# Optimization experiments

Hardware: AMD Instinct MI355X
Metric: run time of the kernel (lower is better)

Reference implementation:

```python
import jax, jax.numpy as jnp
import numpy as np

N = 50000
E = 800000
NUM_KINDS = 100
D_NODE = 64
D_EDGE = 4
D_MSG = 64
L = 3
D_IN = 2 * D_NODE + D_EDGE  # 132


def setup_inputs() -> dict:
    key = jax.random.key(0)
    ks = jax.random.split(key, 20)

    def w(k, shape, fan_in):
        bound = 1.0 / np.sqrt(fan_in)
        return jax.random.uniform(k, shape, jnp.float32, -bound, bound)

    inp = {
        "edge_index": jax.random.randint(ks[0], (2, E), 0, N),
        "node_kind_ids": jax.random.randint(ks[1], (N,), 0, NUM_KINDS),
        "edge_attr": jax.random.normal(ks[2], (E, D_EDGE), jnp.float32),
        # learned params
        "emb": jax.random.normal(ks[3], (NUM_KINDS, D_NODE), jnp.float32),
        # stacked per-layer message MLP params [L, ...]
        "msg_w1": w(ks[4], (L, D_MSG, D_IN), D_IN),
        "msg_b1": w(ks[5], (L, D_MSG), D_IN),
        "msg_w2": w(ks[6], (L, D_MSG, D_MSG), D_MSG),
        "msg_b2": w(ks[7], (L, D_MSG), D_MSG),
        # stacked per-layer GRUCell params (torch layout: [3*d_node, d_in])
        "gru_wih": w(ks[8], (L, 3 * D_NODE, D_MSG), D_NODE),
        "gru_whh": w(ks[9], (L, 3 * D_NODE, D_NODE), D_NODE),
        "gru_bih": w(ks[10], (L, 3 * D_NODE), D_NODE),
        "gru_bhh": w(ks[11], (L, 3 * D_NODE), D_NODE),
        # edge head: Linear(132,64) -> SiLU -> Linear(64,1)
        "head_w1": w(ks[12], (64, D_IN), D_IN),
        "head_b1": w(ks[13], (64,), D_IN),
        "head_w2": w(ks[14], (1, 64), 64),
        "head_b2": w(ks[15], (1,), 64),
    }
    return inp


def reference(edge_index, node_kind_ids, edge_attr, emb,
              msg_w1, msg_b1, msg_w2, msg_b2,
              gru_wih, gru_whh, gru_bih, gru_bhh,
              head_w1, head_b1, head_w2, head_b2):
    src, dst = edge_index[0], edge_index[1]
    h = emb[node_kind_ids]  # [N, d_node]
    n_nodes = h.shape[0]
    for l in range(L):
        x = jnp.concatenate([h[src], h[dst], edge_attr], axis=1)  # [E, 132]
        m = jax.nn.silu(x @ msg_w1[l].T + msg_b1[l]) @ msg_w2[l].T + msg_b2[l]  # [E, d_msg]
        agg = jax.ops.segment_sum(m, dst, num_segments=n_nodes)  # [N, d_msg]
        # torch GRUCell math
        gi = agg @ gru_wih[l].T + gru_bih[l]  # [N, 3*d_node]
        gh = h @ gru_whh[l].T + gru_bhh[l]
        ir, iz, inn = jnp.split(gi, 3, axis=1)
        hr, hz, hn = jnp.split(gh, 3, axis=1)
        r = jax.nn.sigmoid(ir + hr)
        z = jax.nn.sigmoid(iz + hz)
        n = jnp.tanh(inn + r * hn)
        h = (1.0 - z) * n + z * h
    x = jnp.concatenate([h[src], h[dst], edge_attr], axis=1)  # [E, 132]
    logits = (jax.nn.silu(x @ head_w1.T + head_b1) @ head_w2.T + head_b2)[:, 0]
    return jax.nn.sigmoid(logits)  # [E]
```

## Files before the change

### kernel.cpp

```cpp
#include <hip/hip_runtime.h>
#include <hip/hip_bf16.h>


typedef __attribute__((ext_vector_type(8))) short bf16x8;
typedef __attribute__((ext_vector_type(4))) float f32x4;
#define MFMA16(a, b, c) __builtin_amdgcn_mfma_f32_16x16x32_bf16(a, b, c, 0, 0, 0)

#define CHUNK 128
#define XSTRIDE 336
#define MSTRIDE 264
#define HSTRIDE 144
#define SLABSZ 10752
#define HIDSZ  4608

#define WRZST 264
#define WNST  136

__device__ __forceinline__ float fast_sig(float x) { return 1.f / (1.f + __expf(-x)); }
__device__ __forceinline__ float fast_tanh(float x) {
    float ax = fabsf(x);
    float t = __expf(-2.f * ax);
    return copysignf((1.f - t) / (1.f + t), x);
}
__device__ __forceinline__ ushort f2bf(float f) {
    unsigned u = __float_as_uint(f);
    unsigned r = u + 0x7FFF + ((u >> 16) & 1);
    return (ushort)(r >> 16);
}
__device__ __forceinline__ float bf2f(ushort b) {
    return __uint_as_float(((unsigned)b) << 16);
}
__device__ __forceinline__ unsigned pkbf2(float a, float b) {
    unsigned r;
    asm("v_cvt_pk_bf16_f32 %0, %1, %2" : "=v"(r) : "v"(a), "v"(b));
    return r;
}

__global__ void prep_kernel(const float* __restrict__ msg_w1,
                            const float* __restrict__ msg_b1,
                            const float* __restrict__ msg_w2,
                            const float* __restrict__ gru_wih,
                            const float* __restrict__ gru_whh,
                            const float* __restrict__ head_w1,
                            const float* __restrict__ head_b1,
                            const float* __restrict__ head_w2,
                            ushort* __restrict__ Wb1, ushort* __restrict__ Wb2,
                            ushort* __restrict__ Wh1, ushort* __restrict__ Wh2b,
                            ushort* __restrict__ Wrz, ushort* __restrict__ Wni,
                            ushort* __restrict__ Wnh) {
    int t = blockIdx.x * 256 + threadIdx.x;
    if (t < 30720) {
        int l = t / 10240, r = t % 10240, j = r / 160, k = r % 160;
        float v = 0.f;
        if (k < 132) {
            v = msg_w1[l * 8448 + j * 132 + k];
        } else if (k == 132) {
            v = msg_b1[l * 64 + j];
        } else if (k == 133) {
            float b = msg_b1[l * 64 + j];
            v = b - bf2f(f2bf(b));
        }
        Wb1[t] = f2bf(v);
        return;
    }
    t -= 30720;
    if (t < 12288) {
        Wb2[t] = f2bf(msg_w2[t]);
        return;
    }
    t -= 12288;
    if (t < 10240) {
        int j = t / 160, k = t % 160;
        float v = 0.f;
        if (k < 132) {
            v = head_w1[j * 132 + k];
        } else if (k == 132) {
            v = head_b1[j];
        } else if (k == 133) {
            float b = head_b1[j];
            v = b - bf2f(f2bf(b));
        }
        Wh1[t] = f2bf(v);
        return;
    }
    t -= 10240;
    if (t < 1024) {
        int j = t >> 6, k = t & 63;
        Wh2b[t] = (j == 0) ? f2bf(head_w2[k]) : 0;
        return;
    }
    t -= 1024;
    if (t < 49152) {
        int l = t / 16384, r = t % 16384, n = r >> 7, k = r & 127;
        float v = (k < 64) ? gru_wih[l * 12288 + n * 64 + k]
                           : gru_whh[l * 12288 + n * 64 + (k - 64)];
        Wrz[t] = f2bf(v);
        return;
    }
    t -= 49152;
    if (t < 12288) {
        int l = t / 4096, r = t % 4096, j = r >> 6, k = r & 63;
        Wni[t] = f2bf(gru_wih[l * 12288 + (128 + j) * 64 + k]);
        return;
    }
    t -= 12288;
    if (t < 12288) {
        int l = t / 4096, r = t % 4096, j = r >> 6, k = r & 63;
        Wnh[t] = f2bf(gru_whh[l * 12288 + (128 + j) * 64 + k]);
    }
}

__global__ void embed_kernel(float* __restrict__ h, ushort* __restrict__ hb,
                             const float* __restrict__ emb,
                             const int* __restrict__ kinds, int N) {
    int t = blockIdx.x * 256 + threadIdx.x;
    if (t >= N * 64) return;
    int node = t >> 6, d = t & 63;
    float v = emb[kinds[node] * 64 + d];
    h[t] = v;
    hb[t] = f2bf(v);
}

__global__ void hist_kernel(const int* __restrict__ dst, int* __restrict__ deg, int E) {
    int e = blockIdx.x * 256 + threadIdx.x;
    if (e < E) atomicAdd(&deg[dst[e]], 1);
}

__global__ void scan_kernel(const int* __restrict__ deg, int* __restrict__ cursor, int N) {
    __shared__ int sums[1024];
    int tid = threadIdx.x;
    int chunk = (N + 1023) >> 10;
    int lo = tid * chunk, hi = min(lo + chunk, N);
    int s = 0;
    for (int i = lo; i < hi; i++) s += deg[i];
    sums[tid] = s;
    __syncthreads();
    for (int off = 1; off < 1024; off <<= 1) {
        int v = (tid >= off) ? sums[tid - off] : 0;
        __syncthreads();
        sums[tid] += v;
        __syncthreads();
    }
    int run = (tid > 0) ? sums[tid - 1] : 0;
    for (int i = lo; i < hi; i++) {
        cursor[i] = run;
        run += deg[i];
    }
}

__global__ void scatter_kernel(const int* __restrict__ src, const int* __restrict__ dst,
                               const float* __restrict__ ea, int* __restrict__ cursor,
                               int* __restrict__ src_s, int* __restrict__ dst_s,
                               ushort* __restrict__ ea_sb, int E) {
    int e = blockIdx.x * 256 + threadIdx.x;
    if (e >= E) return;
    int d = dst[e];
    int p = atomicAdd(&cursor[d], 1);
    src_s[p] = src[e];
    dst_s[p] = d;
    float4 e4 = ((const float4*)ea)[e];
    ushort4 eb;
    eb.x = f2bf(e4.x); eb.y = f2bf(e4.y); eb.z = f2bf(e4.z); eb.w = f2bf(e4.w);
    ((ushort4*)ea_sb)[p] = eb;
}

__global__ __launch_bounds__(256) void edge_msg_mfma(
    const ushort* __restrict__ hb, const int* __restrict__ src_s,
    const int* __restrict__ dst_s, const ushort* __restrict__ ea_sb,
    const ushort* __restrict__ Wb1l, const ushort* __restrict__ Wb2l,
    const float* __restrict__ b2,
    float* __restrict__ agg, int E, int nchunks) {
    __shared__ char lds[4 * SLABSZ + 4 * HIDSZ];
    int tid = threadIdx.x;
    int w = tid >> 6, lane = tid & 63;
    int quad = lane >> 4, nrow = lane & 15;
    char* slab = lds + w * SLABSZ;
    char* hidb = lds + 4 * SLABSZ + w * HIDSZ;

    bf16x8 wf1[4][5], wf2[4][2];
    float b2v[4];
#pragma unroll
    for (int nt = 0; nt < 4; nt++) {
        int n = nt * 16 + nrow;
#pragma unroll
        for (int ks = 0; ks < 5; ks++)
            wf1[nt][ks] = *(const bf16x8*)(Wb1l + n * 160 + ks * 32 + quad * 8);
#pragma unroll
        for (int ks = 0; ks < 2; ks++)
            wf2[nt][ks] = *(const bf16x8*)(Wb2l + n * 64 + ks * 32 + quad * 8);
        b2v[nt] = b2[n];
    }

    for (int chunk = blockIdx.x; chunk < nchunks; chunk += gridDim.x) {
        int ebase = chunk * CHUNK;
        {
            int el = tid >> 1, half = tid & 1;
            int r = el & 31;
            int ec = min(ebase + el, E - 1);
            int node = half ? dst_s[ec] : src_s[ec];
            const float4* hrow = (const float4*)(hb + (size_t)node * 64);
            float4* xw = (float4*)(slab + r * XSTRIDE + half * 128);
#pragma unroll
            for (int i = 0; i < 8; i++) xw[i] = hrow[i];
            if (half == 0) {
                *(uint2*)(slab + r * XSTRIDE + 256) = *(const uint2*)(ea_sb + (size_t)ec * 4);
            } else {
                uint2 ones2 = {0x3F803F80u, 0u};
                float4 z4 = {0.f, 0.f, 0.f, 0.f};
                *(uint2*)(slab + r * XSTRIDE + 264) = ones2;
                *(float4*)(slab + r * XSTRIDE + 272) = z4;
                *(float4*)(slab + r * XSTRIDE + 288) = z4;
                *(float4*)(slab + r * XSTRIDE + 304) = z4;
            }
        }
        f32x4 acc1[4][2];
#pragma unroll
        for (int nt = 0; nt < 4; nt++) {
            f32x4 z4;
            z4[0] = z4[1] = z4[2] = z4[3] = 0.f;
            acc1[nt][0] = z4;
            acc1[nt][1] = z4;
        }
#pragma unroll
        for (int ks = 0; ks < 5; ks++) {
            bf16x8 xb0 = *(const bf16x8*)(slab + nrow * XSTRIDE + ks * 64 + quad * 16);
            bf16x8 xb1 = *(const bf16x8*)(slab + (16 + nrow) * XSTRIDE + ks * 64 + quad * 16);
#pragma unroll
            for (int nt = 0; nt < 4; nt++) {
                acc1[nt][0] = MFMA16(wf1[nt][ks], xb0, acc1[nt][0]);
                acc1[nt][1] = MFMA16(wf1[nt][ks], xb1, acc1[nt][1]);
            }
        }
#pragma unroll
        for (int nt = 0; nt < 4; nt++)
#pragma unroll
            for (int et = 0; et < 2; et++) {
                f32x4 a = acc1[nt][et];
                float v0 = a[0] * fast_sig(a[0]);
                float v1 = a[1] * fast_sig(a[1]);
                float v2 = a[2] * fast_sig(a[2]);
                float v3 = a[3] * fast_sig(a[3]);
                int er = et * 16 + nrow;
                uint2 pk;
                pk.x = pkbf2(v0, v1);
                pk.y = pkbf2(v2, v3);
                *(uint2*)(hidb + er * HSTRIDE + nt * 32 + quad * 8) = pk;
            }
        f32x4 acc2[2][4];
#pragma unroll
        for (int mt = 0; mt < 2; mt++)
#pragma unroll
            for (int nt = 0; nt < 4; nt++) {
                f32x4 v;
                v[0] = v[1] = v[2] = v[3] = b2v[nt];
                acc2[mt][nt] = v;
            }
#pragma unroll
        for (int ks = 0; ks < 2; ks++) {
            bf16x8 a0 = *(const bf16x8*)(hidb + nrow * HSTRIDE + ks * 64 + quad * 16);
            bf16x8 a1 = *(const bf16x8*)(hidb + (16 + nrow) * HSTRIDE + ks * 64 + quad * 16);
#pragma unroll
            for (int nt = 0; nt < 4; nt++) {
                acc2[0][nt] = MFMA16(a0, wf2[nt][ks], acc2[0][nt]);
                acc2[1][nt] = MFMA16(a1, wf2[nt][ks], acc2[1][nt]);
            }
        }
#pragma unroll
        for (int mt = 0; mt < 2; mt++)
#pragma unroll
            for (int nt = 0; nt < 4; nt++)
#pragma unroll
                for (int rg = 0; rg < 4; rg++) {
                    int rm = mt * 16 + quad * 4 + rg;
                    *(float*)(slab + rm * MSTRIDE + (nt * 16 + nrow) * 4) = acc2[mt][nt][rg];
                }
        {
            int e32 = ebase + w * 32;
            int dmy = dst_s[min(e32 + (lane & 31), E - 1)];
            int limit = min(32, E - e32);
            int nx = __shfl_down(dmy, 1);
            bool tl = ((lane & 31) == 31) || (dmy != nx);
            unsigned long long tm = __ballot(tl);
            float run = 0.f;
#pragma unroll
            for (int i = 0; i < 32; i++) {
                if (i < limit) {
                    run += *(const float*)(slab + i * MSTRIDE + lane * 4);
                    if (((tm >> i) & 1ull) || (i + 1 == limit)) {
                        int di = __shfl(dmy, i);
                        unsafeAtomicAdd(&agg[(size_t)di * 64 + lane], run);
                        run = 0.f;
                    }
                }
            }
        }
    }
}

__global__ __launch_bounds__(256) void head_mfma(
    const ushort* __restrict__ hb, const int* __restrict__ src,
    const int* __restrict__ dst, const float* __restrict__ ea,
    const ushort* __restrict__ Wh1, const ushort* __restrict__ Wh2b,
    const float* __restrict__ hb2p,
    float* __restrict__ out, int E, int nchunks) {
    __shared__ char lds[4 * SLABSZ + 4 * HIDSZ];
    int tid = threadIdx.x;
    int w = tid >> 6, lane = tid & 63;
    int quad = lane >> 4, nrow = lane & 15;
    char* slab = lds + w * SLABSZ;
    char* hidb = lds + 4 * SLABSZ + w * HIDSZ;

    bf16x8 wf1[4][5], wh2[2];
#pragma unroll
    for (int nt = 0; nt < 4; nt++) {
        int n = nt * 16 + nrow;
#pragma unroll
        for (int ks = 0; ks < 5; ks++)
            wf1[nt][ks] = *(const bf16x8*)(Wh1 + n * 160 + ks * 32 + quad * 8);
    }
#pragma unroll
    for (int ks = 0; ks < 2; ks++)
        wh2[ks] = *(const bf16x8*)(Wh2b + nrow * 64 + ks * 32 + quad * 8);
    float hb2 = hb2p[0];

    for (int chunk = blockIdx.x; chunk < nchunks; chunk += gridDim.x) {
        int ebase = chunk * CHUNK;
        {
            int el = tid >> 1, half = tid & 1;
            int r = el & 31;
            int ec = min(ebase + el, E - 1);
            int node = half ? dst[ec] : src[ec];
            const float4* hrow = (const float4*)(hb + (size_t)node * 64);
            float4* xw = (float4*)(slab + r * XSTRIDE + half * 128);
#pragma unroll
            for (int i = 0; i < 8; i++) xw[i] = hrow[i];
            if (half == 0) {
                float4 e4 = ((const float4*)ea)[ec];
                ushort4 eb;
                eb.x = f2bf(e4.x); eb.y = f2bf(e4.y); eb.z = f2bf(e4.z); eb.w = f2bf(e4.w);
                *(ushort4*)(slab + r * XSTRIDE + 256) = eb;
            } else {
                uint2 ones2 = {0x3F803F80u, 0u};
                float4 z4 = {0.f, 0.f, 0.f, 0.f};
                *(uint2*)(slab + r * XSTRIDE + 264) = ones2;
                *(float4*)(slab + r * XSTRIDE + 272) = z4;
                *(float4*)(slab + r * XSTRIDE + 288) = z4;
                *(float4*)(slab + r * XSTRIDE + 304) = z4;
            }
        }
        f32x4 acc1[4][2];
#pragma unroll
        for (int nt = 0; nt < 4; nt++) {
            f32x4 z4;
            z4[0] = z4[1] = z4[2] = z4[3] = 0.f;
            acc1[nt][0] = z4;
            acc1[nt][1] = z4;
        }
#pragma unroll
        for (int ks = 0; ks < 5; ks++) {
            bf16x8 xb0 = *(const bf16x8*)(slab + nrow * XSTRIDE + ks * 64 + quad * 16);
            bf16x8 xb1 = *(const bf16x8*)(slab + (16 + nrow) * XSTRIDE + ks * 64 + quad * 16);
#pragma unroll
            for (int nt = 0; nt < 4; nt++) {
                acc1[nt][0] = MFMA16(wf1[nt][ks], xb0, acc1[nt][0]);
                acc1[nt][1] = MFMA16(wf1[nt][ks], xb1, acc1[nt][1]);
            }
        }
#pragma unroll
        for (int nt = 0; nt < 4; nt++)
#pragma unroll
            for (int et = 0; et < 2; et++) {
                f32x4 a = acc1[nt][et];
                float v0 = a[0] * fast_sig(a[0]);
                float v1 = a[1] * fast_sig(a[1]);
                float v2 = a[2] * fast_sig(a[2]);
                float v3 = a[3] * fast_sig(a[3]);
                int er = et * 16 + nrow;
                uint2 pk;
                pk.x = pkbf2(v0, v1);
                pk.y = pkbf2(v2, v3);
                *(uint2*)(hidb + er * HSTRIDE + nt * 32 + quad * 8) = pk;
            }
        f32x4 acc3[2];
#pragma unroll
        for (int mt = 0; mt < 2; mt++) {
            f32x4 v;
            v[0] = v[1] = v[2] = v[3] = 0.f;
            acc3[mt] = v;
        }
#pragma unroll
        for (int ks = 0; ks < 2; ks++) {
            bf16x8 a0 = *(const bf16x8*)(hidb + nrow * HSTRIDE + ks * 64 + quad * 16);
            bf16x8 a1 = *(const bf16x8*)(hidb + (16 + nrow) * HSTRIDE + ks * 64 + quad * 16);
            acc3[0] = MFMA16(a0, wh2[ks], acc3[0]);
            acc3[1] = MFMA16(a1, wh2[ks], acc3[1]);
        }
        if (nrow == 0) {
#pragma unroll
            for (int mt = 0; mt < 2; mt++)
#pragma unroll
                for (int rg = 0; rg < 4; rg++) {
                    int e = ebase + w * 32 + mt * 16 + quad * 4 + rg;
                    if (e < E) out[e] = fast_sig(acc3[mt][rg] + hb2);
                }
        }
    }
}

__device__ __forceinline__ bf16x8 aggfrag(const float* __restrict__ row, int off) {
    float4 f0 = *(const float4*)(row + off);
    float4 f1 = *(const float4*)(row + off + 4);
    bf16x8 r;
    r[0] = (short)f2bf(f0.x); r[1] = (short)f2bf(f0.y);
    r[2] = (short)f2bf(f0.z); r[3] = (short)f2bf(f0.w);
    r[4] = (short)f2bf(f1.x); r[5] = (short)f2bf(f1.y);
    r[6] = (short)f2bf(f1.z); r[7] = (short)f2bf(f1.w);
    return r;
}

__global__ __launch_bounds__(256) void gru_mfma(
    float* __restrict__ h, ushort* __restrict__ hb, const float* __restrict__ agg,
    const ushort* __restrict__ Wrzg, const ushort* __restrict__ Wnig,
    const ushort* __restrict__ Wnhg,
    const float* __restrict__ bih, const float* __restrict__ bhh, int N) {
    __shared__ char lds[128 * WRZST + 2 * 64 * WNST];
    int tid = threadIdx.x, w = tid >> 6, lane = tid & 63;
    int quad = lane >> 4, nrow = lane & 15;
    char* wrz = lds;
    char* wni = lds + 128 * WRZST;
    char* wnh = wni + 64 * WNST;

    {
        int r = tid >> 1, half = tid & 1;
        const uint4* g = (const uint4*)(Wrzg + r * 128 + half * 64);
        uint4* d = (uint4*)(wrz + r * WRZST + half * 128);
#pragma unroll
        for (int i = 0; i < 8; i++) d[i] = g[i];
        if (tid < 128) {
            const uint4* g2 = (const uint4*)(Wnig + (tid >> 1) * 64 + (tid & 1) * 32);
            uint4* d2 = (uint4*)(wni + (tid >> 1) * WNST + (tid & 1) * 64);
#pragma unroll
            for (int i = 0; i < 4; i++) d2[i] = g2[i];
        } else {
            int t2 = tid - 128;
            const uint4* g2 = (const uint4*)(Wnhg + (t2 >> 1) * 64 + (t2 & 1) * 32);
            uint4* d2 = (uint4*)(wnh + (t2 >> 1) * WNST + (t2 & 1) * 64);
#pragma unroll
            for (int i = 0; i < 4; i++) d2[i] = g2[i];
        }
    }
    __syncthreads();

    int nb0 = blockIdx.x * 128 + w * 32;
    if (nb0 >= N) return;

    float brz[8], bi[4], bhv[4];
#pragma unroll
    for (int nt = 0; nt < 8; nt++) brz[nt] = bih[nt * 16 + nrow] + bhh[nt * 16 + nrow];
#pragma unroll
    for (int nt = 0; nt < 4; nt++) {
        bi[nt] = bih[128 + nt * 16 + nrow];
        bhv[nt] = bhh[128 + nt * 16 + nrow];
    }

    int n0 = min(nb0 + nrow, N - 1);
    int n1 = min(nb0 + 16 + nrow, N - 1);
    const float* ag0 = agg + (size_t)n0 * 64;
    const float* ag1 = agg + (size_t)n1 * 64;
    const ushort* hb0 = hb + (size_t)n0 * 64;
    const ushort* hb1 = hb + (size_t)n1 * 64;

    f32x4 accrz[2][8], acci[2][4], acch[2][4];
#pragma unroll
    for (int nt = 0; nt < 8; nt++) {
        f32x4 v; v[0] = v[1] = v[2] = v[3] = brz[nt];
        accrz[0][nt] = v; accrz[1][nt] = v;
    }
#pragma unroll
    for (int nt = 0; nt < 4; nt++) {
        f32x4 vi; vi[0] = vi[1] = vi[2] = vi[3] = bi[nt];
        acci[0][nt] = vi; acci[1][nt] = vi;
        f32x4 vh; vh[0] = vh[1] = vh[2] = vh[3] = bhv[nt];
        acch[0][nt] = vh; acch[1][nt] = vh;
    }

#pragma unroll
    for (int ks = 0; ks < 4; ks++) {
        bf16x8 a0, a1;
        if (ks < 2) {
            a0 = aggfrag(ag0, ks * 32 + quad * 8);
            a1 = aggfrag(ag1, ks * 32 + quad * 8);
        } else {
            a0 = *(const bf16x8*)(hb0 + (ks - 2) * 32 + quad * 8);
            a1 = *(const bf16x8*)(hb1 + (ks - 2) * 32 + quad * 8);
        }
#pragma unroll
        for (int nt = 0; nt < 8; nt++) {
            bf16x8 b = *(const bf16x8*)(wrz + (nt * 16 + nrow) * WRZST + ks * 64 + quad * 16);
            accrz[0][nt] = MFMA16(a0, b, accrz[0][nt]);
            accrz[1][nt] = MFMA16(a1, b, accrz[1][nt]);
        }
        if (ks < 2) {
#pragma unroll
            for (int nt = 0; nt < 4; nt++) {
                bf16x8 b = *(const bf16x8*)(wni + (nt * 16 + nrow) * WNST + ks * 64 + quad * 16);
                acci[0][nt] = MFMA16(a0, b, acci[0][nt]);
                acci[1][nt] = MFMA16(a1, b, acci[1][nt]);
            }
        } else {
#pragma unroll
            for (int nt = 0; nt < 4; nt++) {
                bf16x8 b = *(const bf16x8*)(wnh + (nt * 16 + nrow) * WNST + (ks - 2) * 64 + quad * 16);
                acch[0][nt] = MFMA16(a0, b, acch[0][nt]);
                acch[1][nt] = MFMA16(a1, b, acch[1][nt]);
            }
        }
    }

#pragma unroll
    for (int mt = 0; mt < 2; mt++)
#pragma unroll
        for (int nt = 0; nt < 4; nt++)
#pragma unroll
            for (int rg = 0; rg < 4; rg++) {
                int node = nb0 + mt * 16 + quad * 4 + rg;
                if (node < N) {
                    int col = nt * 16 + nrow;
                    float r = fast_sig(accrz[mt][nt][rg]);
                    float z = fast_sig(accrz[mt][nt + 4][rg]);
                    float nn = fast_tanh(acci[mt][nt][rg] + r * acch[mt][nt][rg]);
                    size_t idx = (size_t)node * 64 + col;
                    float ho = h[idx];
                    float hnew = (1.f - z) * nn + z * ho;
                    h[idx] = hnew;
                    hb[idx] = f2bf(hnew);
                }
            }
}

extern "C" void kernel_launch(void* const* d_in, const int* in_sizes, int n_in,
                              void* d_out, int out_size, void* d_ws, size_t ws_size,
                              hipStream_t stream) {
    const int* edge_index = (const int*)d_in[0];
    int E = in_sizes[0] / 2;
    const int* src = edge_index;
    const int* dst = edge_index + E;
    const int* kinds = (const int*)d_in[1];
    int N = in_sizes[1];
    const float* edge_attr = (const float*)d_in[2];
    const float* emb = (const float*)d_in[3];
    const float* msg_w1 = (const float*)d_in[4];
    const float* msg_b1 = (const float*)d_in[5];
    const float* msg_w2 = (const float*)d_in[6];
    const float* msg_b2 = (const float*)d_in[7];
    const float* gru_wih = (const float*)d_in[8];
    const float* gru_whh = (const float*)d_in[9];
    const float* gru_bih = (const float*)d_in[10];
    const float* gru_bhh = (const float*)d_in[11];
    const float* head_w1 = (const float*)d_in[12];
    const float* head_b1 = (const float*)d_in[13];
    const float* head_w2 = (const float*)d_in[14];
    const float* head_b2 = (const float*)d_in[15];
    float* out = (float*)d_out;

    char* p = (char*)d_ws;
    float* h = (float*)p;        p += (size_t)N * 64 * 4;
    float* agg = (float*)p;      p += (size_t)N * 64 * 4;
    int* deg = (int*)p;          p += (size_t)N * 4;
    int* cursor = (int*)p;       p += (size_t)N * 4;
    int* src_s = (int*)p;        p += (size_t)E * 4;
    int* dst_s = (int*)p;        p += (size_t)E * 4;
    ushort* hb = (ushort*)p;     p += (size_t)N * 64 * 2;
    ushort* Wb1 = (ushort*)p;    p += 30720 * 2;
    ushort* Wb2 = (ushort*)p;    p += 12288 * 2;
    ushort* Wh1 = (ushort*)p;    p += 10240 * 2;
    ushort* Wh2b = (ushort*)p;   p += 1024 * 2;
    ushort* Wrz = (ushort*)p;    p += 49152 * 2;
    ushort* Wni = (ushort*)p;    p += 12288 * 2;
    ushort* Wnh = (ushort*)p;    p += 12288 * 2;
    ushort* ea_sb = (ushort*)p;  p += (size_t)E * 4 * 2;

    int nchunks = (E + CHUNK - 1) / CHUNK;

    prep_kernel<<<500, 256, 0, stream>>>(msg_w1, msg_b1, msg_w2, gru_wih, gru_whh,
                                         head_w1, head_b1, head_w2,
                                         Wb1, Wb2, Wh1, Wh2b, Wrz, Wni, Wnh);
    embed_kernel<<<(N * 64 + 255) / 256, 256, 0, stream>>>(h, hb, emb, kinds, N);

    hipMemsetAsync(deg, 0, (size_t)N * sizeof(int), stream);
    hist_kernel<<<(E + 255) / 256, 256, 0, stream>>>(dst, deg, E);
    scan_kernel<<<1, 1024, 0, stream>>>(deg, cursor, N);
    scatter_kernel<<<(E + 255) / 256, 256, 0, stream>>>(src, dst, edge_attr, cursor,
                                                        src_s, dst_s, ea_sb, E);

    for (int l = 0; l < 3; l++) {
        hipMemsetAsync(agg, 0, (size_t)N * 64 * sizeof(float), stream);
        edge_msg_mfma<<<512, 256, 0, stream>>>(
            hb, src_s, dst_s, ea_sb,
            Wb1 + l * 10240, Wb2 + l * 4096,
            msg_b2 + l * 64, agg, E, nchunks);
        gru_mfma<<<(N + 127) / 128, 256, 0, stream>>>(
            h, hb, agg, Wrz + l * 16384, Wni + l * 4096, Wnh + l * 4096,
            gru_bih + l * 192, gru_bhh + l * 192, N);
    }
    head_mfma<<<512, 256, 0, stream>>>(hb, src, dst, edge_attr, Wh1, Wh2b,
                                       head_b2, out, E, nchunks);
}
```

Baseline: 671.6 us.

## Raise edge-kernel occupancy by reusing LDS slab and reloading second-layer weights

Result: slower. 706.1 us (+5.1%).

```diff
diff --git a/kernel.cpp b/kernel.cpp
--- a/kernel.cpp
+++ b/kernel.cpp
@@ -11,7 +11,6 @@
 #define MSTRIDE 264
 #define HSTRIDE 144
 #define SLABSZ 10752
-#define HIDSZ  4608
 
 #define WRZST 264
 #define WNST  136
@@ -164,20 +163,19 @@
     ((ushort4*)ea_sb)[p] = eb;
 }
 
-__global__ __launch_bounds__(256) void edge_msg_mfma(
+__global__ __launch_bounds__(256, 3) void edge_msg_mfma(
     const ushort* __restrict__ hb, const int* __restrict__ src_s,
     const int* __restrict__ dst_s, const ushort* __restrict__ ea_sb,
     const ushort* __restrict__ Wb1l, const ushort* __restrict__ Wb2l,
     const float* __restrict__ b2,
     float* __restrict__ agg, int E, int nchunks) {
-    __shared__ char lds[4 * SLABSZ + 4 * HIDSZ];
+    __shared__ char lds[4 * SLABSZ];
     int tid = threadIdx.x;
     int w = tid >> 6, lane = tid & 63;
     int quad = lane >> 4, nrow = lane & 15;
     char* slab = lds + w * SLABSZ;
-    char* hidb = lds + 4 * SLABSZ + w * HIDSZ;
-
-    bf16x8 wf1[4][5], wf2[4][2];
+
+    bf16x8 wf1[4][5];
     float b2v[4];
 #pragma unroll
     for (int nt = 0; nt < 4; nt++) {
@@ -185,9 +183,6 @@
 #pragma unroll
         for (int ks = 0; ks < 5; ks++)
             wf1[nt][ks] = *(const bf16x8*)(Wb1l + n * 160 + ks * 32 + quad * 8);
-#pragma unroll
-        for (int ks = 0; ks < 2; ks++)
-            wf2[nt][ks] = *(const bf16x8*)(Wb2l + n * 64 + ks * 32 + quad * 8);
         b2v[nt] = b2[n];
     }
 
@@ -213,13 +208,12 @@
                 *(float4*)(slab + r * XSTRIDE + 304) = z4;
             }
         }
-        f32x4 acc1[4][2];
-#pragma unroll
-        for (int nt = 0; nt < 4; nt++) {
+        f32x4 acc[8];
+        {
             f32x4 z4;
             z4[0] = z4[1] = z4[2] = z4[3] = 0.f;
-            acc1[nt][0] = z4;
-            acc1[nt][1] = z4;
+#pragma unroll
+            for (int i = 0; i < 8; i++) acc[i] = z4;
         }
 #pragma unroll
         for (int ks = 0; ks < 5; ks++) {
@@ -227,15 +221,15 @@
             bf16x8 xb1 = *(const bf16x8*)(slab + (16 + nrow) * XSTRIDE + ks * 64 + quad * 16);
 #pragma unroll
             for (int nt = 0; nt < 4; nt++) {
-                acc1[nt][0] = MFMA16(wf1[nt][ks], xb0, acc1[nt][0]);
-                acc1[nt][1] = MFMA16(wf1[nt][ks], xb1, acc1[nt][1]);
+                acc[nt * 2 + 0] = MFMA16(wf1[nt][ks], xb0, acc[nt * 2 + 0]);
+                acc[nt * 2 + 1] = MFMA16(wf1[nt][ks], xb1, acc[nt * 2 + 1]);
             }
         }
 #pragma unroll
         for (int nt = 0; nt < 4; nt++)
 #pragma unroll
             for (int et = 0; et < 2; et++) {
-                f32x4 a = acc1[nt][et];
+                f32x4 a = acc[nt * 2 + et];
                 float v0 = a[0] * fast_sig(a[0]);
                 float v1 = a[1] * fast_sig(a[1]);
                 float v2 = a[2] * fast_sig(a[2]);
@@ -244,27 +238,40 @@
                 uint2 pk;
                 pk.x = pkbf2(v0, v1);
                 pk.y = pkbf2(v2, v3);
-                *(uint2*)(hidb + er * HSTRIDE + nt * 32 + quad * 8) = pk;
-            }
-        f32x4 acc2[2][4];
+                *(uint2*)(slab + er * HSTRIDE + nt * 32 + quad * 8) = pk;
+            }
+        bf16x8 ha[2][2];
+#pragma unroll
+        for (int mt = 0; mt < 2; mt++)
+#pragma unroll
+            for (int ks = 0; ks < 2; ks++) {
+                int er = mt * 16 + nrow;
+                ha[mt][ks] = *(const bf16x8*)(slab + er * HSTRIDE + ks * 64 + quad * 16);
+            }
+        const ushort* wb2i = Wb2l;
+        asm volatile("" : "+s"(wb2i));
+        bf16x8 wf2[4][2];
+#pragma unroll
+        for (int nt = 0; nt < 4; nt++)
+#pragma unroll
+            for (int ks = 0; ks < 2; ks++)
+                wf2[nt][ks] =
+                    *(const bf16x8*)(wb2i + (nt * 16 + nrow) * 64 + ks * 32 + quad * 8);
 #pragma unroll
         for (int mt = 0; mt < 2; mt++)
 #pragma unroll
             for (int nt = 0; nt < 4; nt++) {
                 f32x4 v;
                 v[0] = v[1] = v[2] = v[3] = b2v[nt];
-                acc2[mt][nt] = v;
-            }
-#pragma unroll
-        for (int ks = 0; ks < 2; ks++) {
-            bf16x8 a0 = *(const bf16x8*)(hidb + nrow * HSTRIDE + ks * 64 + quad * 16);
-            bf16x8 a1 = *(const bf16x8*)(hidb + (16 + nrow) * HSTRIDE + ks * 64 + quad * 16);
+                acc[mt * 4 + nt] = v;
+            }
+#pragma unroll
+        for (int ks = 0; ks < 2; ks++)
 #pragma unroll
             for (int nt = 0; nt < 4; nt++) {
-                acc2[0][nt] = MFMA16(a0, wf2[nt][ks], acc2[0][nt]);
-                acc2[1][nt] = MFMA16(a1, wf2[nt][ks], acc2[1][nt]);
-            }
-        }
+                acc[0 * 4 + nt] = MFMA16(ha[0][ks], wf2[nt][ks], acc[0 * 4 + nt]);
+                acc[1 * 4 + nt] = MFMA16(ha[1][ks], wf2[nt][ks], acc[1 * 4 + nt]);
+            }
 #pragma unroll
         for (int mt = 0; mt < 2; mt++)
 #pragma unroll
@@ -272,7 +279,8 @@
 #pragma unroll
                 for (int rg = 0; rg < 4; rg++) {
                     int rm = mt * 16 + quad * 4 + rg;
-                    *(float*)(slab + rm * MSTRIDE + (nt * 16 + nrow) * 4) = acc2[mt][nt][rg];
+                    *(float*)(slab + rm * MSTRIDE + (nt * 16 + nrow) * 4) =
+                        acc[mt * 4 + nt][rg];
                 }
         {
             int e32 = ebase + w * 32;
@@ -297,20 +305,19 @@
     }
 }
 
-__global__ __launch_bounds__(256) void head_mfma(
+__global__ __launch_bounds__(256, 3) void head_mfma(
     const ushort* __restrict__ hb, const int* __restrict__ src,
     const int* __restrict__ dst, const float* __restrict__ ea,
     const ushort* __restrict__ Wh1, const ushort* __restrict__ Wh2b,
     const float* __restrict__ hb2p,
     float* __restrict__ out, int E, int nchunks) {
-    __shared__ char lds[4 * SLABSZ + 4 * HIDSZ];
+    __shared__ char lds[4 * SLABSZ];
     int tid = threadIdx.x;
     int w = tid >> 6, lane = tid & 63;
     int quad = lane >> 4, nrow = lane & 15;
     char* slab = lds + w * SLABSZ;
-    char* hidb = lds + 4 * SLABSZ + w * HIDSZ;
-
-    bf16x8 wf1[4][5], wh2[2];
+
+    bf16x8 wf1[4][5];
 #pragma unroll
     for (int nt = 0; nt < 4; nt++) {
         int n = nt * 16 + nrow;
@@ -318,9 +325,6 @@
         for (int ks = 0; ks < 5; ks++)
             wf1[nt][ks] = *(const bf16x8*)(Wh1 + n * 160 + ks * 32 + quad * 8);
     }
-#pragma unroll
-    for (int ks = 0; ks < 2; ks++)
-        wh2[ks] = *(const bf16x8*)(Wh2b + nrow * 64 + ks * 32 + quad * 8);
     float hb2 = hb2p[0];
 
     for (int chunk = blockIdx.x; chunk < nchunks; chunk += gridDim.x) {
@@ -348,13 +352,12 @@
                 *(float4*)(slab + r * XSTRIDE + 304) = z4;
             }
         }
-        f32x4 acc1[4][2];
-#pragma unroll
-        for (int nt = 0; nt < 4; nt++) {
+        f32x4 acc[8];
+        {
             f32x4 z4;
             z4[0] = z4[1] = z4[2] = z4[3] = 0.f;
-            acc1[nt][0] = z4;
-            acc1[nt][1] = z4;
+#pragma unroll
+            for (int i = 0; i < 8; i++) acc[i] = z4;
         }
 #pragma unroll
         for (int ks = 0; ks < 5; ks++) {
@@ -362,15 +365,15 @@
             bf16x8 xb1 = *(const bf16x8*)(slab + (16 + nrow) * XSTRIDE + ks * 64 + quad * 16);
 #pragma unroll
             for (int nt = 0; nt < 4; nt++) {
-                acc1[nt][0] = MFMA16(wf1[nt][ks], xb0, acc1[nt][0]);
-                acc1[nt][1] = MFMA16(wf1[nt][ks], xb1, acc1[nt][1]);
+                acc[nt * 2 + 0] = MFMA16(wf1[nt][ks], xb0, acc[nt * 2 + 0]);
+                acc[nt * 2 + 1] = MFMA16(wf1[nt][ks], xb1, acc[nt * 2 + 1]);
             }
         }
 #pragma unroll
         for (int nt = 0; nt < 4; nt++)
 #pragma unroll
             for (int et = 0; et < 2; et++) {
-                f32x4 a = acc1[nt][et];
+                f32x4 a = acc[nt * 2 + et];
                 float v0 = a[0] * fast_sig(a[0]);
                 float v1 = a[1] * fast_sig(a[1]);
                 float v2 = a[2] * fast_sig(a[2]);
@@ -379,8 +382,23 @@
                 uint2 pk;
                 pk.x = pkbf2(v0, v1);
                 pk.y = pkbf2(v2, v3);
-                *(uint2*)(hidb + er * HSTRIDE + nt * 32 + quad * 8) = pk;
-            }
+                *(uint2*)(slab + er * HSTRIDE + nt * 32 + quad * 8) = pk;
+            }
+        bf16x8 ha[2][2];
+#pragma unroll
+        for (int mt = 0; mt < 2; mt++)
+#pragma unroll
+            for (int ks = 0; ks < 2; ks++) {
+                int er = mt * 16 + nrow;
+                ha[mt][ks] = *(const bf16x8*)(slab + er * HSTRIDE + ks * 64 + quad * 16);
+            }
+        const ushort* wh2i = Wh2b;
+        asm volatile("" : "+s"(wh2i));
+        bf16x8 wh2[2];
+#pragma unroll
+        for (int ks = 0; ks < 2; ks++)
+            wh2[ks] = *(const bf16x8*)(wh2i + nrow * 64 + ks * 32 + quad * 8);
+
         f32x4 acc3[2];
 #pragma unroll
         for (int mt = 0; mt < 2; mt++) {
@@ -390,10 +408,8 @@
         }
 #pragma unroll
         for (int ks = 0; ks < 2; ks++) {
-            bf16x8 a0 = *(const bf16x8*)(hidb + nrow * HSTRIDE + ks * 64 + quad * 16);
-            bf16x8 a1 = *(const bf16x8*)(hidb + (16 + nrow) * HSTRIDE + ks * 64 + quad * 16);
-            acc3[0] = MFMA16(a0, wh2[ks], acc3[0]);
-            acc3[1] = MFMA16(a1, wh2[ks], acc3[1]);
+            acc3[0] = MFMA16(ha[0][ks], wh2[ks], acc3[0]);
+            acc3[1] = MFMA16(ha[1][ks], wh2[ks], acc3[1]);
         }
         if (nrow == 0) {
 #pragma unroll
@@ -595,7 +611,7 @@
 
     for (int l = 0; l < 3; l++) {
         hipMemsetAsync(agg, 0, (size_t)N * 64 * sizeof(float), stream);
-        edge_msg_mfma<<<512, 256, 0, stream>>>(
+        edge_msg_mfma<<<1536, 256, 0, stream>>>(
             hb, src_s, dst_s, ea_sb,
             Wb1 + l * 10240, Wb2 + l * 4096,
             msg_b2 + l * 64, agg, E, nchunks);
@@ -603,6 +619,6 @@
             h, hb, agg, Wrz + l * 16384, Wni + l * 4096, Wnh + l * 4096,
             gru_bih + l * 192, gru_bhh + l * 192, N);
     }
-    head_mfma<<<512, 256, 0, stream>>>(hb, src, dst, edge_attr, Wh1, Wh2b,
-                                       head_b2, out, E, nchunks);
-}
+    head_mfma<<<1536, 256, 0, stream>>>(hb, src, dst, edge_attr, Wh1, Wh2b,
+                                        head_b2, out, E, nchunks);
+}
```
